# Optimization experiments

Hardware: AMD Instinct MI355X
Metric: run time of the kernel (lower is better)

## Reference

```python
import jax, jax.numpy as jnp
import numpy as np

T = 32  # timesteps


def _conv(x, w, pad):
    # x: NCHW, w: OIHW
    return jax.lax.conv_general_dilated(
        x, w, window_strides=(1, 1), padding=[(pad, pad), (pad, pad)],
        dimension_numbers=("NCHW", "OIHW", "NCHW"))


def setup_inputs() -> dict:
    key = jax.random.key(0)
    ks = jax.random.split(key, 10)
    K, D, Cin = 64, 512, 1024
    x = jax.random.normal(ks[0], (256, Cin, 14, 14), dtype=jnp.float32)
    # xavier-ish scales
    redu_w = jax.random.normal(ks[1], (D, Cin, 1, 1), jnp.float32) * (2.0 / (D + Cin)) ** 0.5
    redu_b = jax.random.uniform(ks[2], (D,), jnp.float32)
    share_w = jax.random.normal(ks[3], (K, D, 1, 1), jnp.float32) * (2.0 / (K + D)) ** 0.5
    share_b = jax.random.uniform(ks[4], (K,), jnp.float32)
    fan = K * 9
    U_z = jax.random.normal(ks[5], (K, K, 3, 3), jnp.float32) * (2.0 / (fan + fan)) ** 0.5
    U_r = jax.random.normal(ks[6], (K, K, 3, 3), jnp.float32) * (2.0 / (fan + fan)) ** 0.5
    U_h = jax.random.normal(ks[7], (K, K, 3, 3), jnp.float32) * (2.0 / (fan + fan)) ** 0.5
    lim = (6.0 / (K + D)) ** 0.5
    centers = jax.random.uniform(ks[8], (K, D), jnp.float32, -lim, lim)
    return {"x": x, "redu_w": redu_w, "redu_b": redu_b, "share_w": share_w,
            "share_b": share_b, "U_z": U_z, "U_r": U_r, "U_h": U_h,
            "centers": centers}


def reference(x, redu_w, redu_b, share_w, share_b, U_z, U_r, U_h, centers):
    NT, _, H, W = x.shape
    B = NT // T
    K, D = centers.shape
    # 1x1 channel reduction (with_relu=False)
    xr = _conv(x, redu_w, 0) + redu_b[None, :, None, None]          # (B*T, D, H, W)
    wxb = _conv(xr, share_w, 0) + share_b[None, :, None, None]      # (B*T, K, H, W)
    wxb = wxb.reshape(B, T, K, H, W).transpose(1, 0, 2, 3, 4)       # (T, B, K, H, W)

    def step(h, wt):
        z = jax.nn.sigmoid(wt + _conv(h, U_z, 1))
        r = jax.nn.sigmoid(wt + _conv(h, U_r, 1))
        hh = jnp.tanh(wt + _conv(r * h, U_h, 1))
        h = (1.0 - z) * hh + z * h
        return h, h

    h0 = jnp.zeros((B, K, H, W), x.dtype)
    _, fwd = jax.lax.scan(step, h0, wxb)                 # (T, B, K, H, W)
    _, bwd = jax.lax.scan(step, h0, wxb, reverse=True)   # already re-reversed order
    assign = (fwd + bwd).transpose(1, 0, 2, 3, 4).reshape(B * T, K, H * W)
    assign = jax.nn.softmax(assign, axis=1)              # softmax over centers per pixel

    a = assign.sum(-1, keepdims=True) * centers[None]    # (B*T, K, D)
    xt = xr.reshape(B * T, D, H * W)
    vlad = jnp.einsum("bkp,bdp->bkd", assign, xt) - a    # (B*T, K, D)
    vlad = vlad.reshape(B, T, K, D).sum(axis=1)          # (B, K, D)
    vlad = vlad / jnp.clip(jnp.linalg.norm(vlad, axis=2, keepdims=True), 1e-12)
    vlad = vlad.reshape(B, K * D)
    vlad = vlad / jnp.clip(jnp.linalg.norm(vlad, axis=1, keepdims=True), 1e-12)
    return vlad
```

## Files before the change

### kernel.cpp

```cpp
#include <hip/hip_runtime.h>

#define HW 196
#define WIDTH 14
#define T_STEPS 32
#define KC 64
#define DD 512
#define CIN 1024
#define NFR 256
#define NB 8
#define NCOL (NFR * HW)

using f16x8 = __attribute__((ext_vector_type(8))) _Float16;
using f16x4 = __attribute__((ext_vector_type(4))) _Float16;
using f32x4 = __attribute__((ext_vector_type(4))) float;

__device__ __forceinline__ void gload_lds16(const void* g, void* l) {
  __builtin_amdgcn_global_load_lds(
      (const __attribute__((address_space(1))) void*)g,
      (__attribute__((address_space(3))) void*)l, 16, 0, 0);
}

__device__ __forceinline__ float sigf(float x) {
  return __builtin_amdgcn_rcpf(1.0f + __expf(-x));
}
__device__ __forceinline__ float tanhfast(float x) {
  float e = __expf(2.0f * x);
  return 1.0f - 2.0f * __builtin_amdgcn_rcpf(e + 1.0f);
}

__global__ __launch_bounds__(256)
void cvt_f16(const float* __restrict__ src, _Float16* __restrict__ dst, int nelem) {
  int i = (blockIdx.x * 256 + threadIdx.x) * 4;
  if (i < nelem) {
    float4 v = *reinterpret_cast<const float4*>(src + i);
    f16x4 o;
    o[0] = (_Float16)v.x; o[1] = (_Float16)v.y;
    o[2] = (_Float16)v.z; o[3] = (_Float16)v.w;
    *reinterpret_cast<f16x4*>(dst + i) = o;
  }
}

__global__ __launch_bounds__(256)
void transpose_x(const float* __restrict__ x, _Float16* __restrict__ xh) {
  __shared__ float tile[64][197];
  const int tid = threadIdx.x;
  const int w = tid >> 6, lane = tid & 63;
  const int n = blockIdx.y;
  const int c0 = blockIdx.x * 64;
  const float* src = x + ((size_t)n * CIN + c0) * HW;
  for (int rr = 0; rr < 16; ++rr) {
    int c = w * 16 + rr;
    if (lane < 49) {
      float4 v = *reinterpret_cast<const float4*>(src + (size_t)c * HW + lane * 4);
      tile[c][lane * 4 + 0] = v.x; tile[c][lane * 4 + 1] = v.y;
      tile[c][lane * 4 + 2] = v.z; tile[c][lane * 4 + 3] = v.w;
    }
  }
  __syncthreads();
  _Float16* dst = xh + (size_t)n * HW * CIN + c0;
  #pragma unroll
  for (int pass = 0; pass < 13; ++pass) {
    int p = (tid >> 4) + pass * 16;
    int cg = (tid & 15) * 4;
    if (p < HW) {
      f16x4 v;
      #pragma unroll
      for (int j = 0; j < 4; ++j) v[j] = (_Float16)tile[cg + j][p];
      *reinterpret_cast<f16x4*>(dst + (size_t)p * CIN + cg) = v;
    }
  }
}

template<int BM, int NMT, bool WT>
__global__ __launch_bounds__(256)
void gemm16(const _Float16* __restrict__ A, const _Float16* __restrict__ Bmat,
            const float* __restrict__ bias, float* __restrict__ outC,
            _Float16* __restrict__ outT, int M, int K) {
  constexpr int MF = BM / 32;
  union Smem {
    struct { _Float16 a[BM * 64]; _Float16 b[128 * 64]; } s;
    _Float16 t[WT ? 128 * 132 : 1];
  };
  __shared__ Smem u;

  const int tid = threadIdx.x;
  const int lane = tid & 63;
  const int w = tid >> 6;
  const int wm = w >> 1, wn = w & 1;
  const int l16 = lane & 15, lhi = lane >> 4;
  const int srow = lane >> 3, sslot = lane & 7;
  const int swz = (sslot ^ srow) << 4;
  const int nct = gridDim.x / NMT;
  const int mt = blockIdx.x / nct;
  const int ct = blockIdx.x - mt * nct;
  const int m0 = mt * BM;
  const int col0 = ct * 128;

  f32x4 acc[MF][4];
  #pragma unroll
  for (int i = 0; i < MF; ++i)
    #pragma unroll
    for (int f = 0; f < 4; ++f) acc[i][f] = {0.f, 0.f, 0.f, 0.f};

  for (int k0 = 0; k0 < K; k0 += 64) {
    #pragma unroll
    for (int s = 0; s < BM / 32; ++s) {
      int r = w * (BM / 4) + s * 8;
      gload_lds16((const char*)(A + (size_t)(m0 + r + srow) * K + k0) + swz,
                  (char*)u.s.a + r * 128);
    }
    #pragma unroll
    for (int s = 0; s < 4; ++s) {
      int r = w * 32 + s * 8;
      gload_lds16((const char*)(Bmat + (size_t)(col0 + r + srow) * K + k0) + swz,
                  (char*)u.s.b + r * 128);
    }
    __syncthreads();
    #pragma unroll
    for (int kk = 0; kk < 2; ++kk) {
      f16x8 af[MF];
      #pragma unroll
      for (int i = 0; i < MF; ++i) {
        int row = wm * (MF * 16) + i * 16 + l16;
        af[i] = *reinterpret_cast<const f16x8*>(
            (const char*)u.s.a + row * 128 + ((kk * 64 + lhi * 16) ^ ((row & 7) << 4)));
      }
      #pragma unroll
      for (int f = 0; f < 4; ++f) {
        int row = wn * 64 + f * 16 + l16;
        f16x8 bf = *reinterpret_cast<const f16x8*>(
            (const char*)u.s.b + row * 128 + ((kk * 64 + lhi * 16) ^ ((row & 7) << 4)));
        #pragma unroll
        for (int i = 0; i < MF; ++i)
          acc[i][f] = __builtin_amdgcn_mfma_f32_16x16x32_f16(af[i], bf, acc[i][f], 0, 0, 0);
      }
    }
    __syncthreads();
  }

  if constexpr (!WT) {
    #pragma unroll
    for (int i = 0; i < MF; ++i) {
      int m = m0 + wm * (MF * 16) + i * 16 + lhi * 4;
      float b0 = bias[m], b1 = bias[m + 1], b2 = bias[m + 2], b3 = bias[m + 3];
      #pragma unroll
      for (int f = 0; f < 4; ++f) {
        int col = col0 + wn * 64 + f * 16 + l16;
        float4 o = {acc[i][f][0] + b0, acc[i][f][1] + b1,
                    acc[i][f][2] + b2, acc[i][f][3] + b3};
        *reinterpret_cast<float4*>(outC + (size_t)col * M + m) = o;
      }
    }
  } else {
    #pragma unroll
    for (int i = 0; i < MF; ++i) {
      int ml = wm * (MF * 16) + i * 16 + lhi * 4;
      int m = m0 + ml;
      float b0 = bias[m], b1 = bias[m + 1], b2 = bias[m + 2], b3 = bias[m + 3];
      #pragma unroll
      for (int f = 0; f < 4; ++f) {
        int cl = wn * 64 + f * 16 + l16;
        f16x4 v;
        v[0] = (_Float16)(acc[i][f][0] + b0);
        v[1] = (_Float16)(acc[i][f][1] + b1);
        v[2] = (_Float16)(acc[i][f][2] + b2);
        v[3] = (_Float16)(acc[i][f][3] + b3);
        *reinterpret_cast<f16x4*>((char*)u.t + cl * 264 + ml * 2) = v;
      }
    }
    __syncthreads();
    #pragma unroll
    for (int pass = 0; pass < 16; ++pass) {
      int row = (tid >> 5) + pass * 8;
      int coff = (tid & 31) * 4;
      f16x4 v = *reinterpret_cast<const f16x4*>((const char*)u.t + row * 264 + coff * 2);
      *reinterpret_cast<f16x4*>(outT + (size_t)(col0 + row) * M + m0 + coff) = v;
    }
  }
}

__global__ __launch_bounds__(64)
void format_u(const float* __restrict__ Uz, const float* __restrict__ Ur,
              const float* __restrict__ Uh, _Float16* __restrict__ ufmt) {
  const int f = blockIdx.x;
  const int lane = threadIdx.x;
  const int l16 = lane & 15;
  const float* U;
  int ch, kt;
  if (f < 144) {
    int pair = f / 36, rem = f - pair * 36;
    int mi = rem / 18; kt = rem - mi * 18;
    U = (pair < 2) ? Uz : Ur;
    ch = (pair & 1) * 32 + mi * 16 + l16;
  } else {
    int g = f - 144;
    int pair = g / 36, rem = g - pair * 36;
    int mi = rem / 18; kt = rem - mi * 18;
    U = Uh;
    ch = pair * 32 + mi * 16 + l16;
  }
  const int tap = kt >> 1;
  const int k0 = (kt & 1) * 32 + (lane >> 4) * 8;
  f16x8 v;
  #pragma unroll
  for (int j = 0; j < 8; ++j)
    v[j] = (_Float16)U[(size_t)ch * 576 + (k0 + j) * 9 + tap];
  *reinterpret_cast<f16x8*>(ufmt + (size_t)f * 512 + lane * 8) = v;
}

__global__ __launch_bounds__(512, 2)
void gru_mfma8(const float* __restrict__ wxbc, const _Float16* __restrict__ ufmt,
               _Float16* __restrict__ a_f, _Float16* __restrict__ a_b) {
  __shared__ __align__(16) _Float16 hpad[256 * 64];
  __shared__ __align__(16) _Float16 rhpad[256 * 64];
  __shared__ __align__(16) _Float16 zbuf[208 * 64];
  __shared__ __align__(16) float h32[HW * 68];

  const int tid = threadIdx.x;
  const int lane = tid & 63;
  const int w = tid >> 6;
  const int l16 = lane & 15, lhi = lane >> 4;
  const int chain = blockIdx.x;
  const int b = chain >> 1, dir = chain & 1;
  const int mi = w & 3;
  const int half = w >> 2;
  const int ntb = half * 7;
  const int ntn = half ? 6 : 7;
  const int ch0 = mi * 16 + lhi * 4;
  const int chlo = lhi * 16, chhi = 64 + lhi * 16;

  for (int i = tid; i < 256 * 64; i += 512) { hpad[i] = (_Float16)0.f; rhpad[i] = (_Float16)0.f; }
  for (int i = tid; i < HW * 68; i += 512) h32[i] = 0.0f;
  __syncthreads();

  _Float16* adest = dir ? a_b : a_f;
  const char* hpadB = reinterpret_cast<const char*>(hpad);
  const char* rhpadB = reinterpret_cast<const char*>(rhpad);
  const _Float16* uf = ufmt + (size_t)lane * 8;
  const int fz0 = (mi >> 1) * 36 + (mi & 1) * 18;

  for (int t = 0; t < T_STEPS; ++t) {
    const int tw = dir ? (T_STEPS - 1 - t) : t;
    const float* wtc = wxbc + (size_t)(b * T_STEPS + tw) * HW * KC;

    {
      f16x8 afz[18], afr[18];
      #pragma unroll
      for (int kt = 0; kt < 18; ++kt) {
        afz[kt] = *reinterpret_cast<const f16x8*>(uf + (size_t)(fz0 + kt) * 512);
        afr[kt] = *reinterpret_cast<const f16x8*>(uf + (size_t)(fz0 + 72 + kt) * 512);
      }
      for (int i = 0; i < ntn; ++i) {
        const int nt = ntb + i;
        const int p = nt * 16 + l16;
        const bool act = p < HW;
        const int pc = act ? p : (HW - 1);
        const int py = pc / 14, px_ = pc - py * 14;
        const int base0 = py * 16 + px_;
        const int tb = base0 * 128;
        const int rb0 = tb +       (chlo ^ ((px_ & 7) << 4));
        const int rb1 = tb + 128 + (chlo ^ (((px_ + 1) & 7) << 4));
        const int rb2 = tb + 256 + (chlo ^ (((px_ + 2) & 7) << 4));
        const int rb3 = tb +       (chhi ^ ((px_ & 7) << 4));
        const int rb4 = tb + 128 + (chhi ^ (((px_ + 1) & 7) << 4));
        const int rb5 = tb + 256 + (chhi ^ (((px_ + 2) & 7) << 4));
        const float4 wt4 = *reinterpret_cast<const float4*>(wtc + (size_t)pc * KC + ch0);
        f32x4 az = {0.f, 0.f, 0.f, 0.f};
        f32x4 ar = {0.f, 0.f, 0.f, 0.f};
        #pragma unroll
        for (int kt = 0; kt < 18; ++kt) {
          const int tap = kt >> 1, dy = tap / 3, dx = tap - dy * 3;
          const int base = (kt & 1) ? (dx == 0 ? rb3 : dx == 1 ? rb4 : rb5)
                                    : (dx == 0 ? rb0 : dx == 1 ? rb1 : rb2);
          const f16x8 bf = *reinterpret_cast<const f16x8*>(hpadB + base + dy * 2048);
          az = __builtin_amdgcn_mfma_f32_16x16x32_f16(afz[kt], bf, az, 0, 0, 0);
          ar = __builtin_amdgcn_mfma_f32_16x16x32_f16(afr[kt], bf, ar, 0, 0, 0);
        }
        if (act) {
          const float wta[4] = {wt4.x, wt4.y, wt4.z, wt4.w};
          const float4 hv = *reinterpret_cast<const float4*>(&h32[pc * 68 + ch0]);
          const float hva[4] = {hv.x, hv.y, hv.z, hv.w};
          f16x4 zw, rhw;
          #pragma unroll
          for (int jj = 0; jj < 4; ++jj) {
            float z = sigf(az[jj] + wta[jj]);
            float r = sigf(ar[jj] + wta[jj]);
            zw[jj] = (_Float16)z;
            rhw[jj] = (_Float16)(r * hva[jj]);
          }
          *reinterpret_cast<f16x4*>(reinterpret_cast<char*>(zbuf) +
              p * 128 + ((ch0 * 2) ^ ((p & 7) << 4))) = zw;
          const int ppw = base0 + 17;
          *reinterpret_cast<f16x4*>(reinterpret_cast<char*>(rhpad) +
              ppw * 128 + ((ch0 * 2) ^ ((ppw & 7) << 4))) = rhw;
        }
      }
    }
    __syncthreads();

    {
      _Float16* ad = adest + (size_t)(b * T_STEPS + tw) * HW * KC;
      f16x8 afh[18];
      #pragma unroll
      for (int kt = 0; kt < 18; ++kt)
        afh[kt] = *reinterpret_cast<const f16x8*>(uf + (size_t)(144 + fz0 + kt) * 512);
      for (int i = 0; i < ntn; ++i) {
        const int nt = ntb + i;
        const int p = nt * 16 + l16;
        const bool act = p < HW;
        const int pc = act ? p : (HW - 1);
        const int py = pc / 14, px_ = pc - py * 14;
        const int base0 = py * 16 + px_;
        const int tb = base0 * 128;
        const int rb0 = tb +       (chlo ^ ((px_ & 7) << 4));
        const int rb1 = tb + 128 + (chlo ^ (((px_ + 1) & 7) << 4));
        const int rb2 = tb + 256 + (chlo ^ (((px_ + 2) & 7) << 4));
        const int rb3 = tb +       (chhi ^ ((px_ & 7) << 4));
        const int rb4 = tb + 128 + (chhi ^ (((px_ + 1) & 7) << 4));
        const int rb5 = tb + 256 + (chhi ^ (((px_ + 2) & 7) << 4));
        const float4 wt4 = *reinterpret_cast<const float4*>(wtc + (size_t)pc * KC + ch0);
        f32x4 ah = {0.f, 0.f, 0.f, 0.f};
        #pragma unroll
        for (int kt = 0; kt < 18; ++kt) {
          const int tap = kt >> 1, dy = tap / 3, dx = tap - dy * 3;
          const int base = (kt & 1) ? (dx == 0 ? rb3 : dx == 1 ? rb4 : rb5)
                                    : (dx == 0 ? rb0 : dx == 1 ? rb1 : rb2);
          const f16x8 bf = *reinterpret_cast<const f16x8*>(rhpadB + base + dy * 2048);
          ah = __builtin_amdgcn_mfma_f32_16x16x32_f16(afh[kt], bf, ah, 0, 0, 0);
        }
        if (act) {
          const float wta[4] = {wt4.x, wt4.y, wt4.z, wt4.w};
          const f16x4 zv = *reinterpret_cast<const f16x4*>(
              reinterpret_cast<const char*>(zbuf) + p * 128 + ((ch0 * 2) ^ ((p & 7) << 4)));
          const float4 hv = *reinterpret_cast<const float4*>(&h32[pc * 68 + ch0]);
          const float hva[4] = {hv.x, hv.y, hv.z, hv.w};
          f16x4 hw;
          float hna[4];
          #pragma unroll
          for (int jj = 0; jj < 4; ++jj) {
            float hh = tanhfast(ah[jj] + wta[jj]);
            float z = (float)zv[jj];
            float hn = hh + z * (hva[jj] - hh);
            hna[jj] = hn;
            hw[jj] = (_Float16)hn;
          }
          float4 hn4 = {hna[0], hna[1], hna[2], hna[3]};
          *reinterpret_cast<float4*>(&h32[pc * 68 + ch0]) = hn4;
          const int ppw = base0 + 17;
          *reinterpret_cast<f16x4*>(reinterpret_cast<char*>(hpad) +
              ppw * 128 + ((ch0 * 2) ^ ((ppw & 7) << 4))) = hw;
          *reinterpret_cast<f16x4*>(ad + (size_t)pc * KC + ch0) = hw;
        }
      }
    }
    __syncthreads();
  }
}

__global__ __launch_bounds__(256)
void softmax_kernel(const _Float16* __restrict__ af, const _Float16* __restrict__ ab,
                    float* __restrict__ out) {
  size_t idx = (size_t)blockIdx.x * 256 + threadIdx.x;
  const _Float16* cf = af + idx * KC;
  const _Float16* cb = ab + idx * KC;
  float* co = out + idx * KC;
  float v[KC];
  float mx = -3.4e38f;
  #pragma unroll
  for (int g = 0; g < 8; ++g) {
    f16x8 a = *reinterpret_cast<const f16x8*>(cf + g * 8);
    f16x8 bq = *reinterpret_cast<const f16x8*>(cb + g * 8);
    #pragma unroll
    for (int j = 0; j < 8; ++j) {
      float s = (float)a[j] + (float)bq[j];
      v[g * 8 + j] = s;
      mx = fmaxf(mx, s);
    }
  }
  float ssum = 0.0f;
  #pragma unroll
  for (int k = 0; k < KC; ++k) { v[k] = expf(v[k] - mx); ssum += v[k]; }
  float inv = 1.0f / ssum;
  #pragma unroll
  for (int g = 0; g < 16; ++g) {
    float4 o = {v[g * 4] * inv, v[g * 4 + 1] * inv, v[g * 4 + 2] * inv, v[g * 4 + 3] * inv};
    *reinterpret_cast<float4*>(co + g * 4) = o;
  }
}

__global__ __launch_bounds__(256)
void sreduce_kernel(const float* __restrict__ a, float* __restrict__ S) {
  __shared__ float red[4][64];
  const int seg = blockIdx.x, b = blockIdx.y, tid = threadIdx.x;
  const int k = tid & 63, rg = tid >> 6;
  const float* base = a + (size_t)b * T_STEPS * HW * KC;
  float sum = 0.0f;
  for (int rr = seg * 784 + rg; rr < (seg + 1) * 784; rr += 4)
    sum += base[(size_t)rr * KC + k];
  red[rg][k] = sum;
  __syncthreads();
  if (tid < 64) {
    float s = red[0][k] + red[1][k] + red[2][k] + red[3][k];
    atomicAdd(&S[b * KC + k], s);
  }
}

__global__ __launch_bounds__(256)
void vlad_gemm_kernel(const float* __restrict__ a, const _Float16* __restrict__ xrh,
                      float* __restrict__ Gpart) {
  __shared__ float sA[16][68];
  __shared__ float sX[16][68];
  const int tid = threadIdx.x;
  const int tx = tid & 15, ty = tid >> 4;
  const int d0 = blockIdx.x * 64;
  const int tc = blockIdx.y;
  const int b  = blockIdx.z;
  const int kk = tid & 63, pj = tid >> 6;
  float acc[4][4] = {};

  for (int tt = 0; tt < 8; ++tt) {
    int n = b * T_STEPS + tc * 8 + tt;
    const float* an = a + (size_t)n * HW * KC;
    const _Float16* xn = xrh + (size_t)n * HW * DD;
    for (int p0 = 0; p0 < HW; p0 += 16) {
      __syncthreads();
      #pragma unroll
      for (int j = 0; j < 4; ++j) {
        int pl = pj * 4 + j;
        int p = p0 + pl;
        sA[pl][kk] = (p < HW) ? an[(size_t)p * KC + kk] : 0.0f;
        sX[pl][kk] = (p < HW) ? (float)xn[(size_t)p * DD + d0 + kk] : 0.0f;
      }
      __syncthreads();
      #pragma unroll
      for (int pp = 0; pp < 16; ++pp) {
        float4 av = *reinterpret_cast<const float4*>(&sA[pp][ty * 4]);
        float4 xv = *reinterpret_cast<const float4*>(&sX[pp][tx * 4]);
        float aa[4] = {av.x, av.y, av.z, av.w};
        float xx[4] = {xv.x, xv.y, xv.z, xv.w};
        #pragma unroll
        for (int i = 0; i < 4; ++i)
          #pragma unroll
          for (int j = 0; j < 4; ++j)
            acc[i][j] += aa[i] * xx[j];
      }
    }
  }
  float* gp = Gpart + ((size_t)(tc * NB + b) * KC) * DD;
  #pragma unroll
  for (int i = 0; i < 4; ++i)
    #pragma unroll
    for (int j = 0; j < 4; ++j)
      gp[(ty * 4 + i) * DD + d0 + tx * 4 + j] = acc[i][j];
}

__global__ __launch_bounds__(256)
void finalize1_kernel(const float* __restrict__ Gpart, const float* __restrict__ S,
                      const float* __restrict__ centers, float* __restrict__ out,
                      float* __restrict__ bsum) {
  __shared__ float red[256];
  const int k = blockIdx.x, b = blockIdx.y, tid = threadIdx.x;
  const float sv = S[b * KC + k];
  float vals[2];
  float ss = 0.0f;
  #pragma unroll
  for (int r = 0; r < 2; ++r) {
    int d = tid + r * 256;
    float g = 0.0f;
    #pragma unroll
    for (int tc = 0; tc < 4; ++tc)
      g += Gpart[((size_t)(tc * NB + b) * KC + k) * DD + d];
    float v = g - sv * centers[k * DD + d];
    vals[r] = v; ss += v * v;
  }
  red[tid] = ss; __syncthreads();
  for (int st = 128; st > 0; st >>= 1) {
    if (tid < st) red[tid] += red[tid + st];
    __syncthreads();
  }
  float tot = red[0];
  float inv = 1.0f / fmaxf(sqrtf(tot), 1e-12f);
  #pragma unroll
  for (int r = 0; r < 2; ++r) {
    int d = tid + r * 256;
    out[(size_t)b * KC * DD + k * DD + d] = vals[r] * inv;
  }
  if (tid == 0) atomicAdd(&bsum[b], tot * inv * inv);
}

__global__ __launch_bounds__(256)
void finalize2_kernel(float* __restrict__ out, const float* __restrict__ bsum) {
  int idx = blockIdx.x * 256 + threadIdx.x;
  int b = idx >> 15;
  out[idx] = out[idx] / fmaxf(sqrtf(bsum[b]), 1e-12f);
}

extern "C" void kernel_launch(void* const* d_in, const int* in_sizes, int n_in,
                              void* d_out, int out_size, void* d_ws, size_t ws_size,
                              hipStream_t stream) {
  const float* x       = (const float*)d_in[0];
  const float* redu_w  = (const float*)d_in[1];
  const float* redu_b  = (const float*)d_in[2];
  const float* share_w = (const float*)d_in[3];
  const float* share_b = (const float*)d_in[4];
  const float* Uz      = (const float*)d_in[5];
  const float* Ur      = (const float*)d_in[6];
  const float* Uh      = (const float*)d_in[7];
  const float* centers = (const float*)d_in[8];
  float* out = (float*)d_out;

  float* wxbc = (float*)d_ws;
  _Float16* xh = (_Float16*)(wxbc + (size_t)NCOL * KC);
  _Float16* a_f = xh;
  _Float16* a_b = a_f + (size_t)NFR * HW * KC;
  _Float16* xrh = xh + (size_t)NCOL * CIN;
  float* Gpart = (float*)(xrh + (size_t)NCOL * DD);
  float* S = Gpart + (size_t)4 * NB * KC * DD;
  float* bsum = S + 512;
  _Float16* ufmt = (_Float16*)(bsum + 8);
  _Float16* wh = ufmt + 216 * 512;
  _Float16* swh = wh + (size_t)DD * CIN;
  float* assignc = wxbc;

  hipMemsetAsync(bsum, 0, NB * sizeof(float), stream);
  hipMemsetAsync(S, 0, 512 * sizeof(float), stream);

  cvt_f16<<<dim3(512), 256, 0, stream>>>(redu_w, wh, DD * CIN);
  cvt_f16<<<dim3(32), 256, 0, stream>>>(share_w, swh, KC * DD);
  format_u<<<dim3(216), 64, 0, stream>>>(Uz, Ur, Uh, ufmt);
  transpose_x<<<dim3(16, 256), 256, 0, stream>>>(x, xh);

  gemm16<128, 4, true><<<dim3(392 * 4), 256, 0, stream>>>(
      wh, xh, redu_b, nullptr, xrh, DD, CIN);
  gemm16<64, 1, false><<<dim3(392), 256, 0, stream>>>(
      swh, xrh, share_b, wxbc, nullptr, KC, DD);

  gru_mfma8<<<dim3(16), 512, 0, stream>>>(wxbc, ufmt, a_f, a_b);

  softmax_kernel<<<dim3(196), 256, 0, stream>>>(a_f, a_b, assignc);
  sreduce_kernel<<<dim3(8, 8), 256, 0, stream>>>(assignc, S);
  vlad_gemm_kernel<<<dim3(8, 4, 8), 256, 0, stream>>>(assignc, xrh, Gpart);
  finalize1_kernel<<<dim3(64, 8), 256, 0, stream>>>(Gpart, S, centers, out, bsum);
  finalize2_kernel<<<dim3(1024), 256, 0, stream>>>(out, bsum);
}
```

Before: 864.2 us.

## Store softmax assignments in fp16 and double VLAD GEMM time-chunk split

The softmax kernel now writes assignment probabilities as fp16, using fast exp and reciprocal, and the reduction and VLAD GEMM kernels read fp16. This halves the assignment traffic. The VLAD GEMM grid goes from 4 to 8 time chunks, with 4 frames each, for more parallelism. Finalize now sums 8 partials, and Gpart is moved into the workspace region after the GRU outputs. The cost is lower precision in the assignments and larger partial-sum storage and reads.

```diff
diff --git a/kernel.cpp b/kernel.cpp
--- a/kernel.cpp
+++ b/kernel.cpp
@@ -359,11 +359,11 @@
 
 __global__ __launch_bounds__(256)
 void softmax_kernel(const _Float16* __restrict__ af, const _Float16* __restrict__ ab,
-                    float* __restrict__ out) {
+                    _Float16* __restrict__ out) {
   size_t idx = (size_t)blockIdx.x * 256 + threadIdx.x;
   const _Float16* cf = af + idx * KC;
   const _Float16* cb = ab + idx * KC;
-  float* co = out + idx * KC;
+  _Float16* co = out + idx * KC;
   float v[KC];
   float mx = -3.4e38f;
   #pragma unroll
@@ -379,24 +379,26 @@
   }
   float ssum = 0.0f;
   #pragma unroll
-  for (int k = 0; k < KC; ++k) { v[k] = expf(v[k] - mx); ssum += v[k]; }
-  float inv = 1.0f / ssum;
-  #pragma unroll
-  for (int g = 0; g < 16; ++g) {
-    float4 o = {v[g * 4] * inv, v[g * 4 + 1] * inv, v[g * 4 + 2] * inv, v[g * 4 + 3] * inv};
-    *reinterpret_cast<float4*>(co + g * 4) = o;
-  }
-}
-
-__global__ __launch_bounds__(256)
-void sreduce_kernel(const float* __restrict__ a, float* __restrict__ S) {
+  for (int k = 0; k < KC; ++k) { v[k] = __expf(v[k] - mx); ssum += v[k]; }
+  float inv = __builtin_amdgcn_rcpf(ssum);
+  #pragma unroll
+  for (int g = 0; g < 8; ++g) {
+    f16x8 o;
+    #pragma unroll
+    for (int j = 0; j < 8; ++j) o[j] = (_Float16)(v[g * 8 + j] * inv);
+    *reinterpret_cast<f16x8*>(co + g * 8) = o;
+  }
+}
+
+__global__ __launch_bounds__(256)
+void sreduce_kernel(const _Float16* __restrict__ a, float* __restrict__ S) {
   __shared__ float red[4][64];
   const int seg = blockIdx.x, b = blockIdx.y, tid = threadIdx.x;
   const int k = tid & 63, rg = tid >> 6;
-  const float* base = a + (size_t)b * T_STEPS * HW * KC;
+  const _Float16* base = a + (size_t)b * T_STEPS * HW * KC;
   float sum = 0.0f;
   for (int rr = seg * 784 + rg; rr < (seg + 1) * 784; rr += 4)
-    sum += base[(size_t)rr * KC + k];
+    sum += (float)base[(size_t)rr * KC + k];
   red[rg][k] = sum;
   __syncthreads();
   if (tid < 64) {
@@ -406,7 +408,7 @@
 }
 
 __global__ __launch_bounds__(256)
-void vlad_gemm_kernel(const float* __restrict__ a, const _Float16* __restrict__ xrh,
+void vlad_gemm_kernel(const _Float16* __restrict__ a, const _Float16* __restrict__ xrh,
                       float* __restrict__ Gpart) {
   __shared__ float sA[16][68];
   __shared__ float sX[16][68];
@@ -418,9 +420,9 @@
   const int kk = tid & 63, pj = tid >> 6;
   float acc[4][4] = {};
 
-  for (int tt = 0; tt < 8; ++tt) {
-    int n = b * T_STEPS + tc * 8 + tt;
-    const float* an = a + (size_t)n * HW * KC;
+  for (int tt = 0; tt < 4; ++tt) {
+    int n = b * T_STEPS + tc * 4 + tt;
+    const _Float16* an = a + (size_t)n * HW * KC;
     const _Float16* xn = xrh + (size_t)n * HW * DD;
     for (int p0 = 0; p0 < HW; p0 += 16) {
       __syncthreads();
@@ -428,7 +430,7 @@
       for (int j = 0; j < 4; ++j) {
         int pl = pj * 4 + j;
         int p = p0 + pl;
-        sA[pl][kk] = (p < HW) ? an[(size_t)p * KC + kk] : 0.0f;
+        sA[pl][kk] = (p < HW) ? (float)an[(size_t)p * KC + kk] : 0.0f;
         sX[pl][kk] = (p < HW) ? (float)xn[(size_t)p * DD + d0 + kk] : 0.0f;
       }
       __syncthreads();
@@ -468,7 +470,7 @@
     int d = tid + r * 256;
     float g = 0.0f;
     #pragma unroll
-    for (int tc = 0; tc < 4; ++tc)
+    for (int tc = 0; tc < 8; ++tc)
       g += Gpart[((size_t)(tc * NB + b) * KC + k) * DD + d];
     float v = g - sv * centers[k * DD + d];
     vals[r] = v; ss += v * v;
@@ -510,17 +512,17 @@
   float* out = (float*)d_out;
 
   float* wxbc = (float*)d_ws;
+  _Float16* assignh = (_Float16*)wxbc;
   _Float16* xh = (_Float16*)(wxbc + (size_t)NCOL * KC);
   _Float16* a_f = xh;
   _Float16* a_b = a_f + (size_t)NFR * HW * KC;
+  float* Gpart = (float*)(a_b + (size_t)NFR * HW * KC);
   _Float16* xrh = xh + (size_t)NCOL * CIN;
-  float* Gpart = (float*)(xrh + (size_t)NCOL * DD);
-  float* S = Gpart + (size_t)4 * NB * KC * DD;
+  float* S = (float*)(xrh + (size_t)NCOL * DD);
   float* bsum = S + 512;
   _Float16* ufmt = (_Float16*)(bsum + 8);
   _Float16* wh = ufmt + 216 * 512;
   _Float16* swh = wh + (size_t)DD * CIN;
-  float* assignc = wxbc;
 
   hipMemsetAsync(bsum, 0, NB * sizeof(float), stream);
   hipMemsetAsync(S, 0, 512 * sizeof(float), stream);
@@ -537,9 +539,9 @@
 
   gru_mfma8<<<dim3(16), 512, 0, stream>>>(wxbc, ufmt, a_f, a_b);
 
-  softmax_kernel<<<dim3(196), 256, 0, stream>>>(a_f, a_b, assignc);
-  sreduce_kernel<<<dim3(8, 8), 256, 0, stream>>>(assignc, S);
-  vlad_gemm_kernel<<<dim3(8, 4, 8), 256, 0, stream>>>(assignc, xrh, Gpart);
+  softmax_kernel<<<dim3(196), 256, 0, stream>>>(a_f, a_b, assignh);
+  sreduce_kernel<<<dim3(8, 8), 256, 0, stream>>>(assignh, S);
+  vlad_gemm_kernel<<<dim3(8, 8, 8), 256, 0, stream>>>(assignh, xrh, Gpart);
   finalize1_kernel<<<dim3(64, 8), 256, 0, stream>>>(Gpart, S, centers, out, bsum);
   finalize2_kernel<<<dim3(1024), 256, 0, stream>>>(out, bsum);
 }
```

After: 773.7 us (median of 2 runs). -10.5%, faster.
